# Optimization experiments

Measured on AMD Instinct MI355X. Metric: run time of the kernel, lower is better.

The kernel has to match this reference:

```python
import math
import jax, jax.numpy as jnp
import numpy as np

NEG_INF = -1e9


def maximum_path(neg_cent, text_len, spec_len):
    """Monotonic alignment search (VITS). neg_cent: [B, Ty(spec), Tx(text)].
    Returns hard path [B, Ty, Tx] (float32, 0/1)."""
    B, Ty, Tx = neg_cent.shape
    xs = jnp.arange(Tx)

    # Forward DP over spec frames y; carry = best cumulative value per text pos x.
    def fwd_step(value, inp):
        y, score = inp  # score: [B, Tx]
        diag = jnp.pad(value[:, :-1], ((0, 0), (1, 0)), constant_values=NEG_INF)
        d = diag > value  # move-diagonally indicator for backtracking
        new = score + jnp.maximum(value, diag)
        new = jnp.where(y == 0, jnp.where(xs == 0, score, NEG_INF), new)
        return new, d

    init = jnp.full((B, Tx), NEG_INF, dtype=neg_cent.dtype)
    _, dirs = jax.lax.scan(fwd_step, init,
                           (jnp.arange(Ty), jnp.swapaxes(neg_cent, 0, 1)))
    # dirs: [Ty, B, Tx] bool; dirs[y] compares row y-1 values (as in cython MAS).

    # Backtrack from (spec_len-1, text_len-1) down to y=0.
    def bwd_step(index, inp):
        y, d_row = inp  # index: [B] int32, d_row: [B, Tx]
        active = y < spec_len  # [B]
        row = jnp.where(active[:, None],
                        jax.nn.one_hot(index, Tx, dtype=jnp.float32), 0.0)
        d_at = jnp.take_along_axis(d_row, index[:, None], axis=1)[:, 0]
        move = (index != 0) & ((index == y) | d_at)
        index = jnp.where(active & move, index - 1, index)
        return index, row

    init_idx = text_len - 1
    _, path = jax.lax.scan(bwd_step, init_idx, (jnp.arange(Ty), dirs),
                           reverse=True)
    return jnp.swapaxes(path, 0, 1)  # [B, Ty, Tx]


def setup_inputs() -> dict:
    key = jax.random.key(0)
    ks = jax.random.split(key, 6)
    B, C, Tx, Ty = 8, 192, 512, 2048
    z_p = jax.random.normal(ks[0], (B, C, Ty), dtype=jnp.float32)
    m_p = jax.random.normal(ks[1], (B, C, Tx), dtype=jnp.float32)
    logs_p = 0.1 * jax.random.normal(ks[2], (B, C, Tx), dtype=jnp.float32)
    logs_q = 0.1 * jax.random.normal(ks[3], (B, C, Ty), dtype=jnp.float32)
    text_len = jax.random.randint(ks[4], (B,), Tx * 3 // 4, Tx + 1)
    spec_len = jax.random.randint(ks[5], (B,), Ty * 3 // 4, Ty + 1)
    text_mask = (jnp.arange(Tx)[None, :] < text_len[:, None]).astype(jnp.float32)[:, None, :]
    spec_mask = (jnp.arange(Ty)[None, :] < spec_len[:, None]).astype(jnp.float32)[:, None, :]
    return {"z_p": z_p, "m_p": m_p, "logs_p": logs_p, "logs_q": logs_q,
            "text_mask": text_mask, "spec_mask": spec_mask}


def reference(z_p, m_p, logs_p, logs_q, text_mask, spec_mask):
    text_len = jnp.sum(text_mask, axis=(1, 2)).astype(jnp.int32)  # [B]
    spec_len = jnp.sum(spec_mask, axis=(1, 2)).astype(jnp.int32)  # [B]

    # ---- search_path: neg log-likelihood grid [B, T_spec, T_text] ----
    s_p_sq_r = jnp.exp(-2.0 * logs_p)  # [B, C, Tx]
    nc1 = jnp.sum(-0.5 * math.log(2 * math.pi) - logs_p, axis=1, keepdims=True)  # [B,1,Tx]
    nc2 = jnp.einsum('bct,bcx->btx', -0.5 * z_p * z_p, s_p_sq_r)
    nc3 = jnp.einsum('bct,bcx->btx', z_p, m_p * s_p_sq_r)
    nc4 = jnp.sum(-0.5 * m_p * m_p * s_p_sq_r, axis=1, keepdims=True)  # [B,1,Tx]
    neg_cent = nc1 + nc2 + nc3 + nc4  # [B, Ty, Tx]

    MAS_path = maximum_path(neg_cent, text_len, spec_len)  # [B, Ty, Tx]

    # ---- gather-combine text stats onto spec frames ----
    m_p_a = jnp.einsum('btx,bcx->bct', MAS_path, m_p)      # [B, C, Ty]
    logs_p_a = jnp.einsum('btx,bcx->bct', MAS_path, logs_p)

    # ---- KL divergence loss (VITS) ----
    kl = logs_p_a - logs_q - 0.5 \
        + 0.5 * jnp.square(z_p - m_p_a) * jnp.exp(-2.0 * logs_p_a)
    loss_kl = jnp.sum(kl * spec_mask) / jnp.sum(spec_mask)

    duration = jnp.sum(MAS_path, axis=1)[:, None, :]  # [B, 1, Tx]
    return MAS_path[:, None], m_p_a, logs_p_a, loss_kl, duration
```

## Files before the change

kernel.cpp:

```cpp
#include <hip/hip_runtime.h>
#include <cstdint>
#include <cstddef>

#define BB 8
#define CC 192
#define TXX 512
#define TYY 2048
#define NG_MAX (TYY / 8)

#define NEG_INF (-1e9f)
#define HALF_LOG_2PI 0.9189385332046727f

#define O1 8388608
#define O2 11534336
#define O3 14680064
#define O4 14680065

#define WS_NEG   0
#define WS_S     33554432
#define WS_MSR   36700160
#define WS_BIAS  39845888
#define WS_DIRS  39862272
#define WS_IDX   40910848
#define WS_LENS  40976384
#define WS_PART  40976448

typedef float f32x4 __attribute__((ext_vector_type(4)));

__global__ void k_zero(float* __restrict__ out) {
    int64_t i = (int64_t)blockIdx.x * blockDim.x + threadIdx.x;
    const int64_t n4 = (int64_t)BB * TYY * TXX / 4;
    float4 z4 = make_float4(0.f, 0.f, 0.f, 0.f);
    float4* p4 = (float4*)out;
    for (int64_t k = i; k < n4; k += (int64_t)gridDim.x * blockDim.x) p4[k] = z4;
    if (i < BB * TXX) out[O4 + i] = 0.0f;
}

__global__ void k_prep(const float* __restrict__ logs_p, const float* __restrict__ m_p,
                       float* __restrict__ s, float* __restrict__ msr) {
    int i = blockIdx.x * blockDim.x + threadIdx.x;
    float lp = logs_p[i], m = m_p[i];
    float sv = expf(-2.0f * lp);
    s[i] = sv;
    msr[i] = m * sv;
}

__global__ void k_bias(const float* __restrict__ logs_p, const float* __restrict__ m_p,
                       const float* __restrict__ msr, float* __restrict__ bias) {
    int i = blockIdx.x * blockDim.x + threadIdx.x;
    int b = i >> 9, x = i & (TXX - 1);
    size_t base = (size_t)b * CC * TXX + x;
    const float* lpb = logs_p + base;
    const float* mb  = m_p + base;
    const float* msb = msr + base;
    float acc = 0.f;
#pragma unroll 8
    for (int c = 0; c < CC; ++c)
        acc += -HALF_LOG_2PI - lpb[(size_t)c * TXX] - 0.5f * mb[(size_t)c * TXX] * msb[(size_t)c * TXX];
    bias[i] = acc;
}

__global__ void k_len(const float* __restrict__ tmask, const float* __restrict__ smask,
                      int* __restrict__ lens) {
    __shared__ float red[256];
    int b = blockIdx.x, tid = threadIdx.x;
    float ts = 0.f;
    for (int i = tid; i < TXX; i += 256) ts += tmask[b * TXX + i];
    red[tid] = ts; __syncthreads();
    for (int s = 128; s > 0; s >>= 1) { if (tid < s) red[tid] += red[tid + s]; __syncthreads(); }
    if (tid == 0) lens[b] = (int)(red[0] + 0.5f);
    __syncthreads();
    float ss = 0.f;
    for (int i = tid; i < TYY; i += 256) ss += smask[b * TYY + i];
    red[tid] = ss; __syncthreads();
    for (int s = 128; s > 0; s >>= 1) { if (tid < s) red[tid] += red[tid + s]; __syncthreads(); }
    if (tid == 0) lens[8 + b] = (int)(red[0] + 0.5f);
}

__global__ __launch_bounds__(256) void k_gemm(const float* __restrict__ z,
                                              const float* __restrict__ msr,
                                              const float* __restrict__ sarr,
                                              const float* __restrict__ bias,
                                              const int* __restrict__ lens,
                                              float* __restrict__ neg) {
    int x0 = blockIdx.x * 64, t0 = blockIdx.y * 64, b = blockIdx.z;
    if (x0 >= lens[b] || t0 >= lens[8 + b]) return;

    __shared__ float Zs[16][68], Ms[16][68], Ss[16][68];
    int tid = threadIdx.x;
    int tx = tid & 15, ty = tid >> 4;
    const float* zb = z    + (size_t)b * CC * TYY;
    const float* mb = msr  + (size_t)b * CC * TXX;
    const float* sb = sarr + (size_t)b * CC * TXX;
    int lr = tid >> 4, lc = (tid & 15) * 4;
    float acc[4][4] = {};
    for (int k0 = 0; k0 < CC; k0 += 16) {
        float4 zv = *(const float4*)(zb + (size_t)(k0 + lr) * TYY + t0 + lc);
        float4 mv = *(const float4*)(mb + (size_t)(k0 + lr) * TXX + x0 + lc);
        float4 sv = *(const float4*)(sb + (size_t)(k0 + lr) * TXX + x0 + lc);
        __syncthreads();
        *(float4*)&Zs[lr][lc] = zv;
        *(float4*)&Ms[lr][lc] = mv;
        *(float4*)&Ss[lr][lc] = sv;
        __syncthreads();
#pragma unroll
        for (int k = 0; k < 16; ++k) {
            float4 a4  = *(const float4*)&Zs[k][ty * 4];
            float4 bm4 = *(const float4*)&Ms[k][tx * 4];
            float4 bs4 = *(const float4*)&Ss[k][tx * 4];
            float av[4]  = {a4.x, a4.y, a4.z, a4.w};
            float bmv[4] = {bm4.x, bm4.y, bm4.z, bm4.w};
            float bsv[4] = {bs4.x, bs4.y, bs4.z, bs4.w};
#pragma unroll
            for (int i2 = 0; i2 < 4; ++i2) {
                float a2 = -0.5f * av[i2] * av[i2];
#pragma unroll
                for (int j = 0; j < 4; ++j)
                    acc[i2][j] += av[i2] * bmv[j] + a2 * bsv[j];
            }
        }
    }
    float4 b4 = *(const float4*)(bias + b * TXX + x0 + tx * 4);
    float bv[4] = {b4.x, b4.y, b4.z, b4.w};
#pragma unroll
    for (int i2 = 0; i2 < 4; ++i2) {
        int t = t0 + ty * 4 + i2;
        float4 o;
        o.x = acc[i2][0] + bv[0]; o.y = acc[i2][1] + bv[1];
        o.z = acc[i2][2] + bv[2]; o.w = acc[i2][3] + bv[3];
        *(float4*)(neg + ((size_t)b * TYY + t) * TXX + x0 + tx * 4) = o;
    }
}

#define GLOAD4(DST, PTR, OFF)                                             \
    asm volatile("global_load_dwordx4 %0, %1, off offset:" #OFF           \
                 : "=v"(DST) : "v"(PTR) : "memory")

#define WAIT_VM(N) do {                                                   \
    asm volatile("s_waitcnt vmcnt(" #N ")" ::: "memory");                 \
    __builtin_amdgcn_sched_barrier(0);                                    \
} while (0)

#define LOADG(DST, G) do {                                                \
    const char* p0_ = (const char*)nc4 + (size_t)(G) * 16384 + lane * 32; \
    const char* p2_ = p0_ + 4096;                                         \
    const char* p4_ = p0_ + 8192;                                         \
    const char* p6_ = p0_ + 12288;                                        \
    GLOAD4(DST[0],  p0_, 0);    GLOAD4(DST[1],  p0_, 16);                 \
    GLOAD4(DST[2],  p0_, 2048); GLOAD4(DST[3],  p0_, 2064);               \
    GLOAD4(DST[4],  p2_, 0);    GLOAD4(DST[5],  p2_, 16);                 \
    GLOAD4(DST[6],  p2_, 2048); GLOAD4(DST[7],  p2_, 2064);               \
    GLOAD4(DST[8],  p4_, 0);    GLOAD4(DST[9],  p4_, 16);                 \
    GLOAD4(DST[10], p4_, 2048); GLOAD4(DST[11], p4_, 2064);               \
    GLOAD4(DST[12], p6_, 0);    GLOAD4(DST[13], p6_, 16);                 \
    GLOAD4(DST[14], p6_, 2048); GLOAD4(DST[15], p6_, 2064);               \
} while (0)

#define DPROW(CUR, YB, R) do {                                                \
    int y_ = (YB) + (R);                                                      \
    float s0_ = CUR[2*(R)][0],   s1_ = CUR[2*(R)][1];                         \
    float s2_ = CUR[2*(R)][2],   s3_ = CUR[2*(R)][3];                         \
    float s4_ = CUR[2*(R)+1][0], s5_ = CUR[2*(R)+1][1];                       \
    float s6_ = CUR[2*(R)+1][2], s7_ = CUR[2*(R)+1][3];                       \
    unsigned d_ = 0;                                                          \
    if (y_ == 0) {                                                            \
        if (lane == 0) v[0] = s0_;             \
    } else {                                                                  \
        float pl_ = __int_as_float(__builtin_amdgcn_update_dpp(               \
            0, __float_as_int(v[7]), 0x138, 0xF, 0xF, false));                \
        if (lane == 0) pl_ = NEG_INF;                                         \
        float n0_ = s0_ + fmaxf(v[0], pl_);  if (pl_  > v[0]) d_ |= 1u;       \
        float n1_ = s1_ + fmaxf(v[1], v[0]); if (v[0] > v[1]) d_ |= 2u;       \
        float n2_ = s2_ + fmaxf(v[2], v[1]); if (v[1] > v[2]) d_ |= 4u;       \
        float n3_ = s3_ + fmaxf(v[3], v[2]); if (v[2] > v[3]) d_ |= 8u;       \
        float n4_ = s4_ + fmaxf(v[4], v[3]); if (v[3] > v[4]) d_ |= 16u;      \
        float n5_ = s5_ + fmaxf(v[5], v[4]); if (v[4] > v[5]) d_ |= 32u;      \
        float n6_ = s6_ + fmaxf(v[6], v[5]); if (v[5] > v[6]) d_ |= 64u;      \
        float n7_ = s7_ + fmaxf(v[7], v[6]); if (v[6] > v[7]) d_ |= 128u;     \
        v[0] = n0_; v[1] = n1_; v[2] = n2_; v[3] = n3_;                       \
        v[4] = n4_; v[5] = n5_; v[6] = n6_; v[7] = n7_;                       \
    }                                                                         \
    unsigned t_ = (unsigned)(y_ - 8 * lane);                                  \
    if (t_ < 8u) d_ |= 1u << t_;                 \
    acc |= d_ << (((R) & 3) * 8);                                             \
    if (((R) & 3) == 3) { db32[(y_ >> 2) * 64 + lane] = acc; acc = 0; }       \
} while (0)

#define FWD_ITER(G, CUR, NXT) do {                                \
    int g_ = (G);                                                 \
    if (g_ + 2 < ng) {                                            \
        LOADG(NXT, g_ + 2);                 \
        WAIT_VM(32);                                              \
    } else if (g_ + 1 < ng) {                                     \
        WAIT_VM(16);                                              \
    } else {                                                      \
        WAIT_VM(0);                                               \
    }                                                             \
    int yb_ = 8 * g_;                                             \
    DPROW(CUR, yb_, 0); DPROW(CUR, yb_, 1);                       \
    DPROW(CUR, yb_, 2); DPROW(CUR, yb_, 3);                       \
    DPROW(CUR, yb_, 4); DPROW(CUR, yb_, 5);                       \
    DPROW(CUR, yb_, 6); DPROW(CUR, yb_, 7);                       \
} while (0)

__global__ __launch_bounds__(64, 1) void k_fwd(const float* __restrict__ neg,
                                               const int* __restrict__ lens,
                                               uint32_t* __restrict__ dirs) {
    int b = blockIdx.x, lane = threadIdx.x;
    const float* nc4 = neg + (size_t)b * TYY * TXX;
    uint32_t* db32 = dirs + (size_t)b * (TYY / 4) * 64;
    int slen = lens[8 + b];
    int ng = (slen + 7) >> 3;

    float v[8];
#pragma unroll
    for (int j = 0; j < 8; ++j) v[j] = NEG_INF;
    unsigned acc = 0;

    f32x4 bufA[16], bufB[16], bufC[16];
    LOADG(bufA, 0);
    LOADG(bufB, 1);

    for (int p = 0; p < ng; p += 3) {
        FWD_ITER(p, bufA, bufC);
        if (p + 1 < ng) FWD_ITER(p + 1, bufB, bufA);
        if (p + 2 < ng) FWD_ITER(p + 2, bufC, bufB);
    }
}

__global__ __launch_bounds__(64, 1) void k_bwd(const int* __restrict__ lens,
                                               const uint32_t* __restrict__ dirs,
                                               int* __restrict__ idx_map) {
    int b = blockIdx.x, lane = threadIdx.x;
    const uint32_t* db32 = dirs + (size_t)b * (TYY / 4) * 64;
    int tlen = lens[b], slen = lens[8 + b];

    int idx = tlen - 1;
    int y0 = slen - 1;
    while (y0 >= 0) {
        int nsteps = (y0 + 1 < 32) ? y0 + 1 : 32;
        int y = y0 - lane;
        int yy = (y < 0) ? 0 : y;
        int w0 = (idx >> 5) - 1;
        if (w0 < 0) w0 = 0;
        if (w0 > 14) w0 = 14;
        int qrow = (yy >> 2) * 64;
        int byteoff = (yy & 3) * 8;
        uint32_t lo = 0, hi = 0;
        if (lane < 32) {
#pragma unroll
            for (int k = 0; k < 4; ++k)
                lo |= ((db32[qrow + 4 * w0 + k] >> byteoff) & 0xffu) << (8 * k);
#pragma unroll
            for (int k = 0; k < 4; ++k)
                hi |= ((db32[qrow + 4 * w0 + 4 + k] >> byteoff) & 0xffu) << (8 * k);
        }
        int base = w0 << 5;
        int cap = 0;
#pragma unroll
        for (int j = 0; j < 32; ++j) {
            if (lane == j) cap = idx;
            uint32_t l = (uint32_t)__builtin_amdgcn_readlane((int)lo, j);
            uint32_t h = (uint32_t)__builtin_amdgcn_readlane((int)hi, j);
            int bp = idx - base;
            uint32_t word = (bp & 32) ? h : l;
            int bit = (int)((word >> (bp & 31)) & 1u);
            int move = (int)(idx != 0) & bit;
            idx -= move;
        }
        if (lane < nsteps) idx_map[b * TYY + (y0 - lane)] = cap;
        y0 -= 32;
    }
}

__global__ void k_scatter(const int* __restrict__ lens, const int* __restrict__ idx_map,
                          float* __restrict__ out) {
    int i = blockIdx.x * blockDim.x + threadIdx.x;
    int b = i >> 11, y = i & (TYY - 1);
    if (y < lens[8 + b]) {
        int x = idx_map[i];
        out[(size_t)i * TXX + x] = 1.0f;
        atomicAdd(&out[O4 + b * TXX + x], 1.0f);
    }
}

__global__ __launch_bounds__(256) void k_gather(const float* __restrict__ z_p,
                                                const float* __restrict__ m_p,
                                                const float* __restrict__ logs_p,
                                                const float* __restrict__ logs_q,
                                                const int* __restrict__ lens,
                                                const int* __restrict__ idx_map,
                                                float* __restrict__ out,
                                                float* __restrict__ partials) {
    const int S = BB * CC * TYY / 4;
    int base = blockIdx.x * 256 + threadIdx.x;
    float klsum = 0.f;
#pragma unroll
    for (int r = 0; r < 4; ++r) {
        int i = base + r * S;
        int t = i & (TYY - 1);
        int bc = i >> 11;
        int b = bc / CC;
        float ma = 0.f, la = 0.f;
        if (t < lens[8 + b]) {
            int x = idx_map[b * TYY + t];
            size_t off = (size_t)bc * TXX + x;
            ma = m_p[off];
            la = logs_p[off];
            float zv = z_p[i], lq = logs_q[i];
            float dz = zv - ma;
            klsum += la - lq - 0.5f + 0.5f * dz * dz * expf(-2.0f * la);
        }
        out[O1 + i] = ma;
        out[O2 + i] = la;
    }
    for (int o = 32; o > 0; o >>= 1) klsum += __shfl_down(klsum, o);
    __shared__ float red[4];
    if ((threadIdx.x & 63) == 0) red[threadIdx.x >> 6] = klsum;
    __syncthreads();
    if (threadIdx.x == 0) partials[blockIdx.x] = red[0] + red[1] + red[2] + red[3];
}

__global__ void k_final(const float* __restrict__ partials, const int* __restrict__ lens,
                        float* __restrict__ out) {
    float s = 0.f;
    for (int i = threadIdx.x; i < 3072; i += 256) s += partials[i];
    for (int o = 32; o > 0; o >>= 1) s += __shfl_down(s, o);
    __shared__ float red[4];
    if ((threadIdx.x & 63) == 0) red[threadIdx.x >> 6] = s;
    __syncthreads();
    if (threadIdx.x == 0) {
        float tot = 0.f;
        for (int b = 0; b < 8; ++b) tot += (float)lens[8 + b];
        out[O3] = (red[0] + red[1] + red[2] + red[3]) / tot;
    }
}

extern "C" void kernel_launch(void* const* d_in, const int* in_sizes, int n_in,
                              void* d_out, int out_size, void* d_ws, size_t ws_size,
                              hipStream_t stream) {
    const float* z_p    = (const float*)d_in[0];
    const float* m_p    = (const float*)d_in[1];
    const float* logs_p = (const float*)d_in[2];
    const float* logs_q = (const float*)d_in[3];
    const float* tmask  = (const float*)d_in[4];
    const float* smask  = (const float*)d_in[5];
    float* out = (float*)d_out;
    char* ws = (char*)d_ws;

    float*    neg      = (float*)(ws + WS_NEG);
    float*    sarr     = (float*)(ws + WS_S);
    float*    msr      = (float*)(ws + WS_MSR);
    float*    bias     = (float*)(ws + WS_BIAS);
    uint32_t* dirs     = (uint32_t*)(ws + WS_DIRS);
    int*      idx_map  = (int*)(ws + WS_IDX);
    int*      lens     = (int*)(ws + WS_LENS);
    float*    partials = (float*)(ws + WS_PART);

    hipLaunchKernelGGL(k_zero,    dim3(2048),      dim3(256), 0, stream, out);
    hipLaunchKernelGGL(k_prep,    dim3(3072),      dim3(256), 0, stream, logs_p, m_p, sarr, msr);
    hipLaunchKernelGGL(k_bias,    dim3(16),        dim3(256), 0, stream, logs_p, m_p, msr, bias);
    hipLaunchKernelGGL(k_len,     dim3(8),         dim3(256), 0, stream, tmask, smask, lens);
    hipLaunchKernelGGL(k_gemm,    dim3(8, 32, 8),  dim3(256), 0, stream, z_p, msr, sarr, bias, lens, neg);
    hipLaunchKernelGGL(k_fwd,     dim3(8),         dim3(64),  0, stream, neg, lens, dirs);
    hipLaunchKernelGGL(k_bwd,     dim3(8),         dim3(64),  0, stream, lens, dirs, idx_map);
    hipLaunchKernelGGL(k_scatter, dim3(64),        dim3(256), 0, stream, lens, idx_map, out);
    hipLaunchKernelGGL(k_gather,  dim3(3072),      dim3(256), 0, stream, z_p, m_p, logs_p, logs_q,
                       lens, idx_map, out, partials);
    hipLaunchKernelGGL(k_final,   dim3(1),         dim3(256), 0, stream, partials, lens, out);
}
```

Measured before the change: 564.1 us.

## Fuse MAS backtrack into forward DP kernel and deepen prefetch pipeline

Merges the backtracking kernel into the tail of the forward DP kernel, so the direction bits are consumed by the same blocks right after they are written and one launch disappears. The forward loop now prefetches 4-row groups through four register buffers, three groups ahead, with hand-tuned vmcnt waits replacing the 8-row triple buffering. It also changes the k_bias launch shape to 64 blocks of 64 threads. The hand-counted wait values and the k_bias shape both depend on details not visible here, so correctness risk is moderate.

```diff
diff --git a/kernel.cpp b/kernel.cpp
--- a/kernel.cpp
+++ b/kernel.cpp
@@ -6,7 +6,6 @@
 #define CC 192
 #define TXX 512
 #define TYY 2048
-#define NG_MAX (TYY / 8)
 
 #define NEG_INF (-1e9f)
 #define HALF_LOG_2PI 0.9189385332046727f
@@ -142,18 +141,12 @@
 } while (0)
 
 #define LOADG(DST, G) do {                                                \
-    const char* p0_ = (const char*)nc4 + (size_t)(G) * 16384 + lane * 32; \
+    const char* p0_ = (const char*)nc4 + (size_t)(G) * 8192 + lane * 32;  \
     const char* p2_ = p0_ + 4096;                                         \
-    const char* p4_ = p0_ + 8192;                                         \
-    const char* p6_ = p0_ + 12288;                                        \
-    GLOAD4(DST[0],  p0_, 0);    GLOAD4(DST[1],  p0_, 16);                 \
-    GLOAD4(DST[2],  p0_, 2048); GLOAD4(DST[3],  p0_, 2064);               \
-    GLOAD4(DST[4],  p2_, 0);    GLOAD4(DST[5],  p2_, 16);                 \
-    GLOAD4(DST[6],  p2_, 2048); GLOAD4(DST[7],  p2_, 2064);               \
-    GLOAD4(DST[8],  p4_, 0);    GLOAD4(DST[9],  p4_, 16);                 \
-    GLOAD4(DST[10], p4_, 2048); GLOAD4(DST[11], p4_, 2064);               \
-    GLOAD4(DST[12], p6_, 0);    GLOAD4(DST[13], p6_, 16);                 \
-    GLOAD4(DST[14], p6_, 2048); GLOAD4(DST[15], p6_, 2064);               \
+    GLOAD4(DST[0], p0_, 0);    GLOAD4(DST[1], p0_, 16);                   \
+    GLOAD4(DST[2], p0_, 2048); GLOAD4(DST[3], p0_, 2064);                 \
+    GLOAD4(DST[4], p2_, 0);    GLOAD4(DST[5], p2_, 16);                   \
+    GLOAD4(DST[6], p2_, 2048); GLOAD4(DST[7], p2_, 2064);                 \
 } while (0)
 
 #define DPROW(CUR, YB, R) do {                                                \
@@ -188,88 +181,88 @@
 
 #define FWD_ITER(G, CUR, NXT) do {                                \
     int g_ = (G);                                                 \
-    if (g_ + 2 < ng) {                                            \
-        LOADG(NXT, g_ + 2);                 \
-        WAIT_VM(32);                                              \
-    } else if (g_ + 1 < ng) {                                     \
-        WAIT_VM(16);                                              \
+    if (g_ + 3 < ng4) {                                           \
+        LOADG(NXT, g_ + 3);                 \
+        if (g_ >= 3) { WAIT_VM(27); } else { WAIT_VM(24); }       \
+    } else if (g_ + 2 < ng4) {                                    \
+        WAIT_VM(19);                                              \
+    } else if (g_ + 1 < ng4) {                                    \
+        WAIT_VM(11);                                              \
     } else {                                                      \
-        WAIT_VM(0);                                               \
+        WAIT_VM(3);                                               \
     }                                                             \
-    int yb_ = 8 * g_;                                             \
+    int yb_ = 4 * g_;                                             \
     DPROW(CUR, yb_, 0); DPROW(CUR, yb_, 1);                       \
     DPROW(CUR, yb_, 2); DPROW(CUR, yb_, 3);                       \
-    DPROW(CUR, yb_, 4); DPROW(CUR, yb_, 5);                       \
-    DPROW(CUR, yb_, 6); DPROW(CUR, yb_, 7);                       \
 } while (0)
 
 __global__ __launch_bounds__(64, 1) void k_fwd(const float* __restrict__ neg,
                                                const int* __restrict__ lens,
-                                               uint32_t* __restrict__ dirs) {
+                                               uint32_t* __restrict__ dirs,
+                                               int* __restrict__ idx_map) {
     int b = blockIdx.x, lane = threadIdx.x;
     const float* nc4 = neg + (size_t)b * TYY * TXX;
     uint32_t* db32 = dirs + (size_t)b * (TYY / 4) * 64;
     int slen = lens[8 + b];
-    int ng = (slen + 7) >> 3;
+    int ng4 = (slen + 3) >> 2;
 
     float v[8];
 #pragma unroll
     for (int j = 0; j < 8; ++j) v[j] = NEG_INF;
     unsigned acc = 0;
 
-    f32x4 bufA[16], bufB[16], bufC[16];
+    f32x4 bufA[8], bufB[8], bufC[8], bufD[8];
     LOADG(bufA, 0);
     LOADG(bufB, 1);
-
-    for (int p = 0; p < ng; p += 3) {
-        FWD_ITER(p, bufA, bufC);
-        if (p + 1 < ng) FWD_ITER(p + 1, bufB, bufA);
-        if (p + 2 < ng) FWD_ITER(p + 2, bufC, bufB);
-    }
-}
-
-__global__ __launch_bounds__(64, 1) void k_bwd(const int* __restrict__ lens,
-                                               const uint32_t* __restrict__ dirs,
-                                               int* __restrict__ idx_map) {
-    int b = blockIdx.x, lane = threadIdx.x;
-    const uint32_t* db32 = dirs + (size_t)b * (TYY / 4) * 64;
-    int tlen = lens[b], slen = lens[8 + b];
-
-    int idx = tlen - 1;
-    int y0 = slen - 1;
-    while (y0 >= 0) {
-        int nsteps = (y0 + 1 < 32) ? y0 + 1 : 32;
-        int y = y0 - lane;
-        int yy = (y < 0) ? 0 : y;
-        int w0 = (idx >> 5) - 1;
-        if (w0 < 0) w0 = 0;
-        if (w0 > 14) w0 = 14;
-        int qrow = (yy >> 2) * 64;
-        int byteoff = (yy & 3) * 8;
-        uint32_t lo = 0, hi = 0;
-        if (lane < 32) {
-#pragma unroll
-            for (int k = 0; k < 4; ++k)
-                lo |= ((db32[qrow + 4 * w0 + k] >> byteoff) & 0xffu) << (8 * k);
-#pragma unroll
-            for (int k = 0; k < 4; ++k)
-                hi |= ((db32[qrow + 4 * w0 + 4 + k] >> byteoff) & 0xffu) << (8 * k);
+    LOADG(bufC, 2);
+
+#pragma unroll 1
+    for (int p = 0; p < ng4; p += 4) {
+        FWD_ITER(p, bufA, bufD);
+        if (p + 1 < ng4) FWD_ITER(p + 1, bufB, bufA);
+        if (p + 2 < ng4) FWD_ITER(p + 2, bufC, bufB);
+        if (p + 3 < ng4) FWD_ITER(p + 3, bufD, bufC);
+    }
+
+    WAIT_VM(0);
+    {
+        int tlen = lens[b];
+        int idx = tlen - 1;
+        int y0 = slen - 1;
+        while (y0 >= 0) {
+            int nsteps = (y0 + 1 < 32) ? y0 + 1 : 32;
+            int y = y0 - lane;
+            int yy = (y < 0) ? 0 : y;
+            int w0 = (idx >> 5) - 1;
+            if (w0 < 0) w0 = 0;
+            if (w0 > 14) w0 = 14;
+            int qrow = (yy >> 2) * 64;
+            int byteoff = (yy & 3) * 8;
+            uint32_t lo = 0, hi = 0;
+            if (lane < 32) {
+#pragma unroll
+                for (int k = 0; k < 4; ++k)
+                    lo |= ((db32[qrow + 4 * w0 + k] >> byteoff) & 0xffu) << (8 * k);
+#pragma unroll
+                for (int k = 0; k < 4; ++k)
+                    hi |= ((db32[qrow + 4 * w0 + 4 + k] >> byteoff) & 0xffu) << (8 * k);
+            }
+            int base = w0 << 5;
+            int cap = 0;
+#pragma unroll
+            for (int j = 0; j < 32; ++j) {
+                if (lane == j) cap = idx;
+                uint32_t l = (uint32_t)__builtin_amdgcn_readlane((int)lo, j);
+                uint32_t h = (uint32_t)__builtin_amdgcn_readlane((int)hi, j);
+                int bp = idx - base;
+                uint32_t word = (bp & 32) ? h : l;
+                int bit = (int)((word >> (bp & 31)) & 1u);
+                int move = (int)(idx != 0) & bit;
+                idx -= move;
+            }
+            if (lane < nsteps) idx_map[b * TYY + (y0 - lane)] = cap;
+            y0 -= 32;
         }
-        int base = w0 << 5;
-        int cap = 0;
-#pragma unroll
-        for (int j = 0; j < 32; ++j) {
-            if (lane == j) cap = idx;
-            uint32_t l = (uint32_t)__builtin_amdgcn_readlane((int)lo, j);
-            uint32_t h = (uint32_t)__builtin_amdgcn_readlane((int)hi, j);
-            int bp = idx - base;
-            uint32_t word = (bp & 32) ? h : l;
-            int bit = (int)((word >> (bp & 31)) & 1u);
-            int move = (int)(idx != 0) & bit;
-            idx -= move;
-        }
-        if (lane < nsteps) idx_map[b * TYY + (y0 - lane)] = cap;
-        y0 -= 32;
     }
 }
 
@@ -359,11 +352,10 @@
 
     hipLaunchKernelGGL(k_zero,    dim3(2048),      dim3(256), 0, stream, out);
     hipLaunchKernelGGL(k_prep,    dim3(3072),      dim3(256), 0, stream, logs_p, m_p, sarr, msr);
-    hipLaunchKernelGGL(k_bias,    dim3(16),        dim3(256), 0, stream, logs_p, m_p, msr, bias);
+    hipLaunchKernelGGL(k_bias,    dim3(64),        dim3(64),  0, stream, logs_p, m_p, msr, bias);
     hipLaunchKernelGGL(k_len,     dim3(8),         dim3(256), 0, stream, tmask, smask, lens);
     hipLaunchKernelGGL(k_gemm,    dim3(8, 32, 8),  dim3(256), 0, stream, z_p, msr, sarr, bias, lens, neg);
-    hipLaunchKernelGGL(k_fwd,     dim3(8),         dim3(64),  0, stream, neg, lens, dirs);
-    hipLaunchKernelGGL(k_bwd,     dim3(8),         dim3(64),  0, stream, lens, dirs, idx_map);
+    hipLaunchKernelGGL(k_fwd,     dim3(8),         dim3(64),  0, stream, neg, lens, dirs, idx_map);
     hipLaunchKernelGGL(k_scatter, dim3(64),        dim3(256), 0, stream, lens, idx_map, out);
     hipLaunchKernelGGL(k_gather,  dim3(3072),      dim3(256), 0, stream, z_p, m_p, logs_p, logs_q,
                        lens, idx_map, out, partials);
```

Result: slower. 586.1 us (+3.9%).
